# Kernel tuning notes

Hardware: AMD Instinct MI355X
Metric: run time of the kernel (lower is better)

Reference implementation:

```python
import jax, jax.numpy as jnp
import numpy as np

N_NODES = 50000
N_EDGES = 800000
HID = 96

def setup_inputs() -> dict:
    key = jax.random.key(0)
    ks = jax.random.split(key, 12)
    s = 1.0 / np.sqrt(HID)
    return {
        "x_feat": jax.random.normal(ks[0], (N_NODES, HID), jnp.float32),
        "bases": jax.random.normal(ks[1], (N_EDGES, HID), jnp.float32) * 0.1,
        "W_pre": jax.random.normal(ks[2], (HID, HID), jnp.float32) * s,
        "b_pre": jax.random.normal(ks[3], (HID,), jnp.float32) * s,
        "W1": jax.random.normal(ks[4], (HID, HID), jnp.float32) * s,
        "b1": jax.random.normal(ks[5], (HID,), jnp.float32) * s,
        "W2": jax.random.normal(ks[6], (HID, HID), jnp.float32) * s,
        "b2": jax.random.normal(ks[7], (HID,), jnp.float32) * s,
        "src": jax.random.randint(ks[8], (N_EDGES,), 0, N_NODES, jnp.int32),
        "dst": jax.random.randint(ks[9], (N_EDGES,), 0, N_NODES, jnp.int32),
    }

def _gelu(x):
    return jax.nn.gelu(x, approximate=False)  # torch nn.GELU default = erf

def reference(x_feat, bases, W_pre, b_pre, W1, b1, W2, b2, src, dst):
    n = x_feat.shape[0]
    # pre_ffn: Linear + GELU on node features
    h = _gelu(x_feat @ W_pre + b_pre)                      # [N, H]
    # update_all(u_mul_e('x','v'), sum): gather src feats, weight by edge bases, scatter-add to dst
    msg = h[src] * bases                                   # [E, H]
    aggr = jax.ops.segment_sum(msg, dst, num_segments=n)   # [N, H]
    # dropout is identity in eval mode (rate=0)
    x = x_feat + aggr                                      # residual 1
    y = _gelu(_gelu(x @ W1 + b1) @ W2 + b2)                # ffn (no batch norm)
    return x + y                                           # residual 2
```

## Files before the change

### kernel.cpp

```cpp
#include <hip/hip_runtime.h>

#define NODES 50000
#define EDGES 800000
#define H 96
#define CAP 64

typedef float floatx4 __attribute__((ext_vector_type(4)));
typedef unsigned short ushort8 __attribute__((ext_vector_type(8)));
typedef __bf16 bf16x8 __attribute__((ext_vector_type(8)));

static __device__ __forceinline__ unsigned short f2b(float f) {
    unsigned int u = __float_as_uint(f);
    u = u + 0x7fffu + ((u >> 16) & 1u);
    return (unsigned short)(u >> 16);
}
static __device__ __forceinline__ float b2f(unsigned short u) {
    return __uint_as_float(((unsigned int)u) << 16);
}
static __device__ __forceinline__ float gelu_erf(float x) {
    return 0.5f * x * (1.0f + erff(x * 0.70710678118654752f));
}
static __device__ __forceinline__ bf16x8 pack_bf8(floatx4 a, floatx4 b) {
    union { ushort8 u; bf16x8 v; } r;
    #pragma unroll
    for (int j = 0; j < 4; ++j) { r.u[j] = f2b(a[j]); r.u[4 + j] = f2b(b[j]); }
    return r.v;
}

__global__ __launch_bounds__(256) void gemm96_pre(
    const float* __restrict__ A,
    const float* __restrict__ W,
    const float* __restrict__ bias,
    unsigned short* __restrict__ outp,
    int* __restrict__ cursor,
    int* __restrict__ wctr,
    int nStrips)
{
    const int g = blockIdx.x * 256 + threadIdx.x;
    if (g < NODES) cursor[g] = g * CAP;
    if (g == 0) *wctr = 0;

    __shared__ unsigned short Wt[96][104];
    const int tid = threadIdx.x;
    #pragma unroll
    for (int j = 0; j < 36; ++j) {
        const int f = tid + 256 * j;
        const int k = f / 96, n = f - k * 96;
        Wt[n][k] = f2b(W[f]);
    }
    __syncthreads();

    const int lane = tid & 63;
    const int quad = lane >> 4;
    const int l16  = lane & 15;

    bf16x8 Bf[3][6];
    float  bv[6];
    #pragma unroll
    for (int ks = 0; ks < 3; ++ks)
        #pragma unroll
        for (int nt = 0; nt < 6; ++nt)
            Bf[ks][nt] = *(const bf16x8*)(&Wt[nt * 16 + l16][ks * 32 + quad * 8]);
    #pragma unroll
    for (int nt = 0; nt < 6; ++nt) bv[nt] = bias[nt * 16 + l16];

    const int gwave  = (blockIdx.x * 256 + tid) >> 6;
    const int nWaves = (gridDim.x * 256) >> 6;

    for (int strip = gwave; strip < nStrips; strip += nWaves) {
        const int row0 = strip * 16;
        const float* Ap = A + (size_t)(row0 + l16) * H + quad * 8;

        bf16x8 Af[3];
        #pragma unroll
        for (int ks = 0; ks < 3; ++ks) {
            const floatx4 a0 = *(const floatx4*)(Ap + ks * 32);
            const floatx4 a1 = *(const floatx4*)(Ap + ks * 32 + 4);
            Af[ks] = pack_bf8(a0, a1);
        }

        floatx4 acc[6];
        #pragma unroll
        for (int nt = 0; nt < 6; ++nt) acc[nt] = (floatx4){0.f, 0.f, 0.f, 0.f};
        #pragma unroll
        for (int ks = 0; ks < 3; ++ks)
            #pragma unroll
            for (int nt = 0; nt < 6; ++nt)
                acc[nt] = __builtin_amdgcn_mfma_f32_16x16x32_bf16(Af[ks], Bf[ks][nt], acc[nt], 0, 0, 0);

        #pragma unroll
        for (int nt = 0; nt < 6; ++nt) {
            const int col = nt * 16 + l16;
            #pragma unroll
            for (int r = 0; r < 4; ++r) {
                const int row = row0 + quad * 4 + r;
                outp[(size_t)row * H + col] = f2b(gelu_erf(acc[nt][r] + bv[nt]));
            }
        }
    }
}

__global__ __launch_bounds__(256) void build_csr2(
    const int* __restrict__ dst, const int* __restrict__ src,
    int* __restrict__ cursor, int2* __restrict__ csr)
{
    const int e = blockIdx.x * 256 + threadIdx.x;
    if (e < EDGES) {
        const int d = dst[e];
        const int p = atomicAdd(&cursor[d], 1);
        if (p < d * CAP + CAP) {
            int2 es; es.x = e; es.y = src[e];
            csr[p] = es;
        }
    }
}

__global__ __launch_bounds__(256, 2) void gather_ffn(
    const unsigned short* __restrict__ h,
    const float* __restrict__ bases,
    const int2* __restrict__ csr,
    const int* __restrict__ cursor,
    const float* __restrict__ x_feat,
    const float* __restrict__ W1, const float* __restrict__ b1,
    const float* __restrict__ W2, const float* __restrict__ b2,
    float* __restrict__ outp,
    int* __restrict__ wctr,
    int nStrips)
{
    __shared__ unsigned short Wt1[96][104];
    __shared__ unsigned short Wt2[96][104];
    __shared__ float          Xb[4][16][100];
    __shared__ unsigned short Tt[4][16][120];

    const int tid = threadIdx.x;
    #pragma unroll
    for (int j = 0; j < 36; ++j) {
        const int f = tid + 256 * j;
        const int k = f / 96, n = f - k * 96;
        Wt1[n][k] = f2b(W1[f]);
        Wt2[n][k] = f2b(W2[f]);
    }
    __syncthreads();

    const int lane = tid & 63;
    const int quad = lane >> 4;
    const int l16  = lane & 15;
    const int w    = tid >> 6;
    const int nd   = lane >> 2;
    const int seg  = lane & 3;
    const int c0   = seg * 24;

    float bv1[6], bv2[6];
    #pragma unroll
    for (int nt = 0; nt < 6; ++nt) {
        bv1[nt] = b1[nt * 16 + l16];
        bv2[nt] = b2[nt * 16 + l16];
    }

    for (;;) {
        int s;
        if (lane == 0) s = atomicAdd(wctr, 1);
        s = __shfl(s, 0);
        if (s >= nStrips) break;
        const int row0 = s * 16;

        const int node = row0 + nd;
        const int i0 = node * CAP;
        const int i1 = cursor[node];

        float acc[24];
        #pragma unroll
        for (int j = 0; j < 24; ++j) acc[j] = 0.f;
        for (int i = i0; i < i1; ++i) {
            const int2 es = csr[i];
            const float* bp = bases + (size_t)es.x * H + c0;
            const unsigned short* hp = h + (size_t)es.y * H + c0;
            floatx4 b[6]; ushort8 hv[3];
            #pragma unroll
            for (int j = 0; j < 6; ++j) b[j] = *(const floatx4*)(bp + 4 * j);
            #pragma unroll
            for (int j = 0; j < 3; ++j) hv[j] = *(const ushort8*)(hp + 8 * j);
            #pragma unroll
            for (int j = 0; j < 24; ++j)
                acc[j] = fmaf(b[j >> 2][j & 3], b2f(hv[j >> 3][j & 7]), acc[j]);
        }
        const float* xp = x_feat + (size_t)node * H + c0;
        #pragma unroll
        for (int j = 0; j < 6; ++j) {
            const floatx4 xv = *(const floatx4*)(xp + 4 * j);
            #pragma unroll
            for (int t = 0; t < 4; ++t) acc[4 * j + t] += xv[t];
        }
        #pragma unroll
        for (int j = 0; j < 6; ++j) {
            floatx4 v;
            #pragma unroll
            for (int t = 0; t < 4; ++t) v[t] = acc[4 * j + t];
            *(floatx4*)(&Xb[w][nd][c0 + 4 * j]) = v;
        }

        bf16x8 Af[3];
        #pragma unroll
        for (int ks = 0; ks < 3; ++ks) {
            const floatx4 a0 = *(const floatx4*)(&Xb[w][l16][ks * 32 + quad * 8]);
            const floatx4 a1 = *(const floatx4*)(&Xb[w][l16][ks * 32 + quad * 8 + 4]);
            Af[ks] = pack_bf8(a0, a1);
        }
        floatx4 facc[6];
        #pragma unroll
        for (int nt = 0; nt < 6; ++nt) facc[nt] = (floatx4){0.f, 0.f, 0.f, 0.f};
        #pragma unroll
        for (int ks = 0; ks < 3; ++ks)
            #pragma unroll
            for (int nt = 0; nt < 6; ++nt) {
                const bf16x8 Bf1 = *(const bf16x8*)(&Wt1[nt * 16 + l16][ks * 32 + quad * 8]);
                facc[nt] = __builtin_amdgcn_mfma_f32_16x16x32_bf16(Af[ks], Bf1, facc[nt], 0, 0, 0);
            }
        #pragma unroll
        for (int nt = 0; nt < 6; ++nt)
            #pragma unroll
            for (int r = 0; r < 4; ++r)
                Tt[w][quad * 4 + r][nt * 16 + l16] = f2b(gelu_erf(facc[nt][r] + bv1[nt]));

        bf16x8 Tf[3];
        #pragma unroll
        for (int ks = 0; ks < 3; ++ks)
            Tf[ks] = *(const bf16x8*)(&Tt[w][l16][ks * 32 + quad * 8]);
        #pragma unroll
        for (int nt = 0; nt < 6; ++nt) facc[nt] = (floatx4){0.f, 0.f, 0.f, 0.f};
        #pragma unroll
        for (int ks = 0; ks < 3; ++ks)
            #pragma unroll
            for (int nt = 0; nt < 6; ++nt) {
                const bf16x8 Bf2 = *(const bf16x8*)(&Wt2[nt * 16 + l16][ks * 32 + quad * 8]);
                facc[nt] = __builtin_amdgcn_mfma_f32_16x16x32_bf16(Tf[ks], Bf2, facc[nt], 0, 0, 0);
            }
        #pragma unroll
        for (int nt = 0; nt < 6; ++nt) {
            const int col = nt * 16 + l16;
            #pragma unroll
            for (int r = 0; r < 4; ++r) {
                const int row = row0 + quad * 4 + r;
                outp[(size_t)row * H + col] = Xb[w][quad * 4 + r][col]
                                            + gelu_erf(facc[nt][r] + bv2[nt]);
            }
        }
    }
}

extern "C" void kernel_launch(void* const* d_in, const int* in_sizes, int n_in,
                              void* d_out, int out_size, void* d_ws, size_t ws_size,
                              hipStream_t stream)
{
    const float* x_feat = (const float*)d_in[0];
    const float* bases  = (const float*)d_in[1];
    const float* W_pre  = (const float*)d_in[2];
    const float* b_pre  = (const float*)d_in[3];
    const float* W1     = (const float*)d_in[4];
    const float* b1     = (const float*)d_in[5];
    const float* W2     = (const float*)d_in[6];
    const float* b2     = (const float*)d_in[7];
    const int* src = (const int*)d_in[8];
    const int* dst = (const int*)d_in[9];

    char* ws = (char*)d_ws;
    int*            cursor = (int*)(ws);
    int*            wctr   = (int*)(ws + 200704);
    int2*           csr2   = (int2*)(ws + 1048576);
    unsigned short* h_bf   = (unsigned short*)(ws + 27262976);
    float*          out    = (float*)d_out;

    const int nStrips = NODES / 16;

    gemm96_pre<<<512, 256, 0, stream>>>(x_feat, W_pre, b_pre, h_bf, cursor, wctr, nStrips);
    build_csr2<<<(EDGES + 255) / 256, 256, 0, stream>>>(dst, src, cursor, csr2);
    gather_ffn<<<512, 256, 0, stream>>>(
        h_bf, bases, csr2, cursor, x_feat, W1, b1, W2, b2, out, wctr, nStrips);
}
```

Baseline: 569.9 us.

## Gather directly in MFMA operand layout, shrink scratch LDS, raise occupancy

The gather now assigns each lane the columns matching its MFMA A-fragment (node = l16, columns quad*8 + ks*32). The aggregated residual can then be packed straight into bf16 operands, with no LDS round trip. Per-wave scratch is reduced to one 3.5KB buffer that is reused for the residual transpose (done in two halves) and the XOR-swizzled GELU intermediate. That frees enough LDS for launch bounds of 3 blocks per SM and a 768-block grid. The edge loop is unrolled by two to expose more outstanding loads, and it clamps the edge count to CAP. The cost is more complex register use and some extra LDS stores and reads for the residual.

Result: faster. 557.7 us (-2.1%).

```diff
diff --git a/kernel.cpp b/kernel.cpp
--- a/kernel.cpp
+++ b/kernel.cpp
@@ -20,11 +20,17 @@
 static __device__ __forceinline__ float gelu_erf(float x) {
     return 0.5f * x * (1.0f + erff(x * 0.70710678118654752f));
 }
-static __device__ __forceinline__ bf16x8 pack_bf8(floatx4 a, floatx4 b) {
+static __device__ __forceinline__ bf16x8 pack_bf8(const float* a) {
     union { ushort8 u; bf16x8 v; } r;
     #pragma unroll
-    for (int j = 0; j < 4; ++j) { r.u[j] = f2b(a[j]); r.u[4 + j] = f2b(b[j]); }
+    for (int j = 0; j < 8; ++j) r.u[j] = f2b(a[j]);
     return r.v;
+}
+static __device__ __forceinline__ floatx4 vec4(const float* a) {
+    floatx4 v;
+    #pragma unroll
+    for (int j = 0; j < 4; ++j) v[j] = a[j];
+    return v;
 }
 
 __global__ __launch_bounds__(256) void gemm96_pre(
@@ -74,9 +80,12 @@
         bf16x8 Af[3];
         #pragma unroll
         for (int ks = 0; ks < 3; ++ks) {
+            float tmp[8];
             const floatx4 a0 = *(const floatx4*)(Ap + ks * 32);
             const floatx4 a1 = *(const floatx4*)(Ap + ks * 32 + 4);
-            Af[ks] = pack_bf8(a0, a1);
+            #pragma unroll
+            for (int j = 0; j < 4; ++j) { tmp[j] = a0[j]; tmp[4 + j] = a1[j]; }
+            Af[ks] = pack_bf8(tmp);
         }
 
         floatx4 acc[6];
@@ -115,7 +124,7 @@
     }
 }
 
-__global__ __launch_bounds__(256, 2) void gather_ffn(
+__global__ __launch_bounds__(256, 3) void gather_ffn(
     const unsigned short* __restrict__ h,
     const float* __restrict__ bases,
     const int2* __restrict__ csr,
@@ -129,8 +138,7 @@
 {
     __shared__ unsigned short Wt1[96][104];
     __shared__ unsigned short Wt2[96][104];
-    __shared__ float          Xb[4][16][100];
-    __shared__ unsigned short Tt[4][16][120];
+    __shared__ __align__(16) char Scr[4][3584];
 
     const int tid = threadIdx.x;
     #pragma unroll
@@ -146,9 +154,8 @@
     const int quad = lane >> 4;
     const int l16  = lane & 15;
     const int w    = tid >> 6;
-    const int nd   = lane >> 2;
-    const int seg  = lane & 3;
-    const int c0   = seg * 24;
+    float*          Sf = (float*)Scr[w];
+    unsigned short* St = (unsigned short*)Scr[w];
 
     float bv1[6], bv2[6];
     #pragma unroll
@@ -156,6 +163,9 @@
         bv1[nt] = b1[nt * 16 + l16];
         bv2[nt] = b2[nt * 16 + l16];
     }
+
+    const int wsw = quad << 3;
+    const int rsw = ((l16 >> 2) & 3) << 3;
 
     for (;;) {
         int s;
@@ -164,48 +174,97 @@
         if (s >= nStrips) break;
         const int row0 = s * 16;
 
-        const int node = row0 + nd;
+        const int node = row0 + l16;
         const int i0 = node * CAP;
-        const int i1 = cursor[node];
+        int i1 = cursor[node];
+        i1 = min(i1, i0 + CAP);
 
         float acc[24];
         #pragma unroll
         for (int j = 0; j < 24; ++j) acc[j] = 0.f;
-        for (int i = i0; i < i1; ++i) {
-            const int2 es = csr[i];
-            const float* bp = bases + (size_t)es.x * H + c0;
-            const unsigned short* hp = h + (size_t)es.y * H + c0;
-            floatx4 b[6]; ushort8 hv[3];
-            #pragma unroll
-            for (int j = 0; j < 6; ++j) b[j] = *(const floatx4*)(bp + 4 * j);
-            #pragma unroll
-            for (int j = 0; j < 3; ++j) hv[j] = *(const ushort8*)(hp + 8 * j);
-            #pragma unroll
-            for (int j = 0; j < 24; ++j)
-                acc[j] = fmaf(b[j >> 2][j & 3], b2f(hv[j >> 3][j & 7]), acc[j]);
-        }
-        const float* xp = x_feat + (size_t)node * H + c0;
-        #pragma unroll
-        for (int j = 0; j < 6; ++j) {
-            const floatx4 xv = *(const floatx4*)(xp + 4 * j);
-            #pragma unroll
-            for (int t = 0; t < 4; ++t) acc[4 * j + t] += xv[t];
-        }
-        #pragma unroll
-        for (int j = 0; j < 6; ++j) {
-            floatx4 v;
-            #pragma unroll
-            for (int t = 0; t < 4; ++t) v[t] = acc[4 * j + t];
-            *(floatx4*)(&Xb[w][nd][c0 + 4 * j]) = v;
-        }
+
+        int i = i0;
+        for (; i + 1 < i1; i += 2) {
+            const int2 ea = csr[i];
+            const int2 eb = csr[i + 1];
+            const float* bpa = bases + (size_t)ea.x * H + quad * 8;
+            const float* bpb = bases + (size_t)eb.x * H + quad * 8;
+            const unsigned short* hpa = h + (size_t)ea.y * H + quad * 8;
+            const unsigned short* hpb = h + (size_t)eb.y * H + quad * 8;
+            floatx4 ba[6], bb[6]; ushort8 hva[3], hvb[3];
+            #pragma unroll
+            for (int ks = 0; ks < 3; ++ks) {
+                ba[2*ks]   = *(const floatx4*)(bpa + ks * 32);
+                ba[2*ks+1] = *(const floatx4*)(bpa + ks * 32 + 4);
+                hva[ks]    = *(const ushort8*)(hpa + ks * 32);
+                bb[2*ks]   = *(const floatx4*)(bpb + ks * 32);
+                bb[2*ks+1] = *(const floatx4*)(bpb + ks * 32 + 4);
+                hvb[ks]    = *(const ushort8*)(hpb + ks * 32);
+            }
+            #pragma unroll
+            for (int ks = 0; ks < 3; ++ks)
+                #pragma unroll
+                for (int j = 0; j < 8; ++j) {
+                    acc[ks*8+j] = fmaf(ba[2*ks + (j>>2)][j&3], b2f(hva[ks][j]), acc[ks*8+j]);
+                    acc[ks*8+j] = fmaf(bb[2*ks + (j>>2)][j&3], b2f(hvb[ks][j]), acc[ks*8+j]);
+                }
+        }
+        if (i < i1) {
+            const int2 ea = csr[i];
+            const float* bpa = bases + (size_t)ea.x * H + quad * 8;
+            const unsigned short* hpa = h + (size_t)ea.y * H + quad * 8;
+            #pragma unroll
+            for (int ks = 0; ks < 3; ++ks) {
+                const floatx4 b0 = *(const floatx4*)(bpa + ks * 32);
+                const floatx4 b1v = *(const floatx4*)(bpa + ks * 32 + 4);
+                const ushort8 hv = *(const ushort8*)(hpa + ks * 32);
+                #pragma unroll
+                for (int j = 0; j < 4; ++j) {
+                    acc[ks*8+j]   = fmaf(b0[j],  b2f(hv[j]),     acc[ks*8+j]);
+                    acc[ks*8+4+j] = fmaf(b1v[j], b2f(hv[4+j]),   acc[ks*8+4+j]);
+                }
+            }
+        }
+
+        const float* xp = x_feat + (size_t)node * H + quad * 8;
+        #pragma unroll
+        for (int ks = 0; ks < 3; ++ks) {
+            const floatx4 x0 = *(const floatx4*)(xp + ks * 32);
+            const floatx4 x1 = *(const floatx4*)(xp + ks * 32 + 4);
+            #pragma unroll
+            for (int j = 0; j < 4; ++j) {
+                acc[ks*8+j]   += x0[j];
+                acc[ks*8+4+j] += x1[j];
+            }
+        }
+
+        *(floatx4*)&Sf[l16 * 52 + quad * 8]     = vec4(&acc[0]);
+        *(floatx4*)&Sf[l16 * 52 + quad * 8 + 4] = vec4(&acc[4]);
+        if (quad < 2) {
+            *(floatx4*)&Sf[l16 * 52 + 32 + quad * 8]     = vec4(&acc[8]);
+            *(floatx4*)&Sf[l16 * 52 + 32 + quad * 8 + 4] = vec4(&acc[12]);
+        }
+        float res[24];
+        #pragma unroll
+        for (int nt = 0; nt < 3; ++nt)
+            #pragma unroll
+            for (int r = 0; r < 4; ++r)
+                res[nt*4+r] = Sf[(quad*4+r) * 52 + nt*16 + l16];
+        if (quad >= 2) {
+            *(floatx4*)&Sf[l16 * 52 + (quad-2) * 8]     = vec4(&acc[8]);
+            *(floatx4*)&Sf[l16 * 52 + (quad-2) * 8 + 4] = vec4(&acc[12]);
+        }
+        *(floatx4*)&Sf[l16 * 52 + 16 + quad * 8]     = vec4(&acc[16]);
+        *(floatx4*)&Sf[l16 * 52 + 16 + quad * 8 + 4] = vec4(&acc[20]);
+        #pragma unroll
+        for (int nt = 3; nt < 6; ++nt)
+            #pragma unroll
+            for (int r = 0; r < 4; ++r)
+                res[nt*4+r] = Sf[(quad*4+r) * 52 + nt*16 + l16 - 48];
 
         bf16x8 Af[3];
         #pragma unroll
-        for (int ks = 0; ks < 3; ++ks) {
-            const floatx4 a0 = *(const floatx4*)(&Xb[w][l16][ks * 32 + quad * 8]);
-            const floatx4 a1 = *(const floatx4*)(&Xb[w][l16][ks * 32 + quad * 8 + 4]);
-            Af[ks] = pack_bf8(a0, a1);
-        }
+        for (int ks = 0; ks < 3; ++ks) Af[ks] = pack_bf8(&acc[ks * 8]);
         floatx4 facc[6];
         #pragma unroll
         for (int nt = 0; nt < 6; ++nt) facc[nt] = (floatx4){0.f, 0.f, 0.f, 0.f};
@@ -216,16 +275,18 @@
                 const bf16x8 Bf1 = *(const bf16x8*)(&Wt1[nt * 16 + l16][ks * 32 + quad * 8]);
                 facc[nt] = __builtin_amdgcn_mfma_f32_16x16x32_bf16(Af[ks], Bf1, facc[nt], 0, 0, 0);
             }
+
         #pragma unroll
         for (int nt = 0; nt < 6; ++nt)
             #pragma unroll
             for (int r = 0; r < 4; ++r)
-                Tt[w][quad * 4 + r][nt * 16 + l16] = f2b(gelu_erf(facc[nt][r] + bv1[nt]));
-
+                St[(quad*4+r) * 112 + ((nt*16 + l16) ^ wsw)] =
+                    f2b(gelu_erf(facc[nt][r] + bv1[nt]));
         bf16x8 Tf[3];
         #pragma unroll
         for (int ks = 0; ks < 3; ++ks)
-            Tf[ks] = *(const bf16x8*)(&Tt[w][l16][ks * 32 + quad * 8]);
+            Tf[ks] = *(const bf16x8*)(&St[l16 * 112 + ((ks*32 + quad*8) ^ rsw)]);
+
         #pragma unroll
         for (int nt = 0; nt < 6; ++nt) facc[nt] = (floatx4){0.f, 0.f, 0.f, 0.f};
         #pragma unroll
@@ -241,8 +302,7 @@
             #pragma unroll
             for (int r = 0; r < 4; ++r) {
                 const int row = row0 + quad * 4 + r;
-                outp[(size_t)row * H + col] = Xb[w][quad * 4 + r][col]
-                                            + gelu_erf(facc[nt][r] + bv2[nt]);
+                outp[(size_t)row * H + col] = res[nt*4+r] + gelu_erf(facc[nt][r] + bv2[nt]);
             }
         }
     }
@@ -274,6 +334,6 @@
 
     gemm96_pre<<<512, 256, 0, stream>>>(x_feat, W_pre, b_pre, h_bf, cursor, wctr, nStrips);
     build_csr2<<<(EDGES + 255) / 256, 256, 0, stream>>>(dst, src, cursor, csr2);
-    gather_ffn<<<512, 256, 0, stream>>>(
+    gather_ffn<<<768, 256, 0, stream>>>(
         h_bf, bases, csr2, cursor, x_feat, W1, b1, W2, b2, out, wctr, nStrips);
 }
```

## Split fused gather+FFN into a high-occupancy gather kernel and a separate FFN kernel

Applied to the files above, without the earlier changes.

The fused gather_ffn kernel is split in two. A new gather_nodes kernel uses 12 threads per node, each handling 8 features, with two edges per loop iteration and a launch bound of 8 blocks per CU, to raise memory-level parallelism on the random edge gathers. It writes the residual x to a global fp32 workspace, which ffn_dual then reads back, adding an extra write and read of the node features. The FFN stage swaps the atomic work counter for a static grid-stride loop and XOR-swizzles the intermediate shared tile to avoid bank conflicts.

Measured after the change: 535.1 us. 6.1% less time.

```diff
diff --git a/kernel.cpp b/kernel.cpp
--- a/kernel.cpp
+++ b/kernel.cpp
@@ -20,10 +20,10 @@
 static __device__ __forceinline__ float gelu_erf(float x) {
     return 0.5f * x * (1.0f + erff(x * 0.70710678118654752f));
 }
-static __device__ __forceinline__ bf16x8 pack_bf8(floatx4 a, floatx4 b) {
+static __device__ __forceinline__ bf16x8 pack_bf8(const float* a) {
     union { ushort8 u; bf16x8 v; } r;
     #pragma unroll
-    for (int j = 0; j < 4; ++j) { r.u[j] = f2b(a[j]); r.u[4 + j] = f2b(b[j]); }
+    for (int j = 0; j < 8; ++j) r.u[j] = f2b(a[j]);
     return r.v;
 }
 
@@ -33,12 +33,10 @@
     const float* __restrict__ bias,
     unsigned short* __restrict__ outp,
     int* __restrict__ cursor,
-    int* __restrict__ wctr,
     int nStrips)
 {
     const int g = blockIdx.x * 256 + threadIdx.x;
     if (g < NODES) cursor[g] = g * CAP;
-    if (g == 0) *wctr = 0;
 
     __shared__ unsigned short Wt[96][104];
     const int tid = threadIdx.x;
@@ -74,9 +72,12 @@
         bf16x8 Af[3];
         #pragma unroll
         for (int ks = 0; ks < 3; ++ks) {
+            float tmp[8];
             const floatx4 a0 = *(const floatx4*)(Ap + ks * 32);
             const floatx4 a1 = *(const floatx4*)(Ap + ks * 32 + 4);
-            Af[ks] = pack_bf8(a0, a1);
+            #pragma unroll
+            for (int j = 0; j < 4; ++j) { tmp[j] = a0[j]; tmp[4 + j] = a1[j]; }
+            Af[ks] = pack_bf8(tmp);
         }
 
         floatx4 acc[6];
@@ -115,22 +116,80 @@
     }
 }
 
-__global__ __launch_bounds__(256, 2) void gather_ffn(
+__global__ __launch_bounds__(256, 8) void gather_nodes(
     const unsigned short* __restrict__ h,
     const float* __restrict__ bases,
     const int2* __restrict__ csr,
     const int* __restrict__ cursor,
     const float* __restrict__ x_feat,
+    float* __restrict__ xb)
+{
+    const int t = blockIdx.x * 256 + threadIdx.x;
+    const int n = t / 12;
+    if (n >= NODES) return;
+    const int seg = t - n * 12;
+    const int so8 = seg * 8;
+    const int i0 = n * CAP;
+    const int i1 = min(cursor[n], i0 + CAP);
+
+    floatx4 acc0 = (floatx4){0.f, 0.f, 0.f, 0.f};
+    floatx4 acc1 = (floatx4){0.f, 0.f, 0.f, 0.f};
+
+    int i = i0;
+    for (; i + 1 < i1; i += 2) {
+        const int2 ea = csr[i];
+        const int2 eb = csr[i + 1];
+        const size_t eoa = (size_t)ea.x * H + so8;
+        const size_t eob = (size_t)eb.x * H + so8;
+        const floatx4 ba0 = *(const floatx4*)(bases + eoa);
+        const floatx4 ba1 = *(const floatx4*)(bases + eoa + 4);
+        const ushort8 hva = *(const ushort8*)(h + (size_t)ea.y * H + so8);
+        const floatx4 bb0 = *(const floatx4*)(bases + eob);
+        const floatx4 bb1 = *(const floatx4*)(bases + eob + 4);
+        const ushort8 hvb = *(const ushort8*)(h + (size_t)eb.y * H + so8);
+        #pragma unroll
+        for (int j = 0; j < 4; ++j) {
+            acc0[j] = fmaf(ba0[j], b2f(hva[j]),     acc0[j]);
+            acc1[j] = fmaf(ba1[j], b2f(hva[4 + j]), acc1[j]);
+        }
+        #pragma unroll
+        for (int j = 0; j < 4; ++j) {
+            acc0[j] = fmaf(bb0[j], b2f(hvb[j]),     acc0[j]);
+            acc1[j] = fmaf(bb1[j], b2f(hvb[4 + j]), acc1[j]);
+        }
+    }
+    if (i < i1) {
+        const int2 ea = csr[i];
+        const size_t eoa = (size_t)ea.x * H + so8;
+        const floatx4 ba0 = *(const floatx4*)(bases + eoa);
+        const floatx4 ba1 = *(const floatx4*)(bases + eoa + 4);
+        const ushort8 hva = *(const ushort8*)(h + (size_t)ea.y * H + so8);
+        #pragma unroll
+        for (int j = 0; j < 4; ++j) {
+            acc0[j] = fmaf(ba0[j], b2f(hva[j]),     acc0[j]);
+            acc1[j] = fmaf(ba1[j], b2f(hva[4 + j]), acc1[j]);
+        }
+    }
+
+    const size_t no = (size_t)n * H + so8;
+    const floatx4 x0 = *(const floatx4*)(x_feat + no);
+    const floatx4 x1 = *(const floatx4*)(x_feat + no + 4);
+    #pragma unroll
+    for (int j = 0; j < 4; ++j) { acc0[j] += x0[j]; acc1[j] += x1[j]; }
+    *(floatx4*)(xb + no)     = acc0;
+    *(floatx4*)(xb + no + 4) = acc1;
+}
+
+__global__ __launch_bounds__(256) void ffn_dual(
+    const float* __restrict__ A,
     const float* __restrict__ W1, const float* __restrict__ b1,
     const float* __restrict__ W2, const float* __restrict__ b2,
     float* __restrict__ outp,
-    int* __restrict__ wctr,
     int nStrips)
 {
     __shared__ unsigned short Wt1[96][104];
     __shared__ unsigned short Wt2[96][104];
-    __shared__ float          Xb[4][16][100];
-    __shared__ unsigned short Tt[4][16][120];
+    __shared__ unsigned short St[4][16][112];
 
     const int tid = threadIdx.x;
     #pragma unroll
@@ -146,9 +205,6 @@
     const int quad = lane >> 4;
     const int l16  = lane & 15;
     const int w    = tid >> 6;
-    const int nd   = lane >> 2;
-    const int seg  = lane & 3;
-    const int c0   = seg * 24;
 
     float bv1[6], bv2[6];
     #pragma unroll
@@ -157,54 +213,25 @@
         bv2[nt] = b2[nt * 16 + l16];
     }
 
-    for (;;) {
-        int s;
-        if (lane == 0) s = atomicAdd(wctr, 1);
-        s = __shfl(s, 0);
-        if (s >= nStrips) break;
-        const int row0 = s * 16;
-
-        const int node = row0 + nd;
-        const int i0 = node * CAP;
-        const int i1 = cursor[node];
-
-        float acc[24];
-        #pragma unroll
-        for (int j = 0; j < 24; ++j) acc[j] = 0.f;
-        for (int i = i0; i < i1; ++i) {
-            const int2 es = csr[i];
-            const float* bp = bases + (size_t)es.x * H + c0;
-            const unsigned short* hp = h + (size_t)es.y * H + c0;
-            floatx4 b[6]; ushort8 hv[3];
-            #pragma unroll
-            for (int j = 0; j < 6; ++j) b[j] = *(const floatx4*)(bp + 4 * j);
-            #pragma unroll
-            for (int j = 0; j < 3; ++j) hv[j] = *(const ushort8*)(hp + 8 * j);
-            #pragma unroll
-            for (int j = 0; j < 24; ++j)
-                acc[j] = fmaf(b[j >> 2][j & 3], b2f(hv[j >> 3][j & 7]), acc[j]);
-        }
-        const float* xp = x_feat + (size_t)node * H + c0;
-        #pragma unroll
-        for (int j = 0; j < 6; ++j) {
-            const floatx4 xv = *(const floatx4*)(xp + 4 * j);
-            #pragma unroll
-            for (int t = 0; t < 4; ++t) acc[4 * j + t] += xv[t];
-        }
-        #pragma unroll
-        for (int j = 0; j < 6; ++j) {
-            floatx4 v;
-            #pragma unroll
-            for (int t = 0; t < 4; ++t) v[t] = acc[4 * j + t];
-            *(floatx4*)(&Xb[w][nd][c0 + 4 * j]) = v;
-        }
+    const int wsw = quad << 3;
+    const int rsw = (l16 >> 2) << 3;
+
+    const int gwave  = (blockIdx.x * 256 + tid) >> 6;
+    const int nWaves = (gridDim.x * 256) >> 6;
+
+    for (int strip = gwave; strip < nStrips; strip += nWaves) {
+        const int row0 = strip * 16;
+        const float* Ap = A + (size_t)(row0 + l16) * H + quad * 8;
 
         bf16x8 Af[3];
         #pragma unroll
         for (int ks = 0; ks < 3; ++ks) {
-            const floatx4 a0 = *(const floatx4*)(&Xb[w][l16][ks * 32 + quad * 8]);
-            const floatx4 a1 = *(const floatx4*)(&Xb[w][l16][ks * 32 + quad * 8 + 4]);
-            Af[ks] = pack_bf8(a0, a1);
+            float tmp[8];
+            const floatx4 a0 = *(const floatx4*)(Ap + ks * 32);
+            const floatx4 a1 = *(const floatx4*)(Ap + ks * 32 + 4);
+            #pragma unroll
+            for (int j = 0; j < 4; ++j) { tmp[j] = a0[j]; tmp[4 + j] = a1[j]; }
+            Af[ks] = pack_bf8(tmp);
         }
         floatx4 facc[6];
         #pragma unroll
@@ -216,16 +243,18 @@
                 const bf16x8 Bf1 = *(const bf16x8*)(&Wt1[nt * 16 + l16][ks * 32 + quad * 8]);
                 facc[nt] = __builtin_amdgcn_mfma_f32_16x16x32_bf16(Af[ks], Bf1, facc[nt], 0, 0, 0);
             }
+
         #pragma unroll
         for (int nt = 0; nt < 6; ++nt)
             #pragma unroll
             for (int r = 0; r < 4; ++r)
-                Tt[w][quad * 4 + r][nt * 16 + l16] = f2b(gelu_erf(facc[nt][r] + bv1[nt]));
-
+                St[w][quad * 4 + r][(nt * 16 + l16) ^ wsw] =
+                    f2b(gelu_erf(facc[nt][r] + bv1[nt]));
         bf16x8 Tf[3];
         #pragma unroll
         for (int ks = 0; ks < 3; ++ks)
-            Tf[ks] = *(const bf16x8*)(&Tt[w][l16][ks * 32 + quad * 8]);
+            Tf[ks] = *(const bf16x8*)(&St[w][l16][(ks * 32 + quad * 8) ^ rsw]);
+
         #pragma unroll
         for (int nt = 0; nt < 6; ++nt) facc[nt] = (floatx4){0.f, 0.f, 0.f, 0.f};
         #pragma unroll
@@ -241,8 +270,8 @@
             #pragma unroll
             for (int r = 0; r < 4; ++r) {
                 const int row = row0 + quad * 4 + r;
-                outp[(size_t)row * H + col] = Xb[w][quad * 4 + r][col]
-                                            + gelu_erf(facc[nt][r] + bv2[nt]);
+                const size_t o = (size_t)row * H + col;
+                outp[o] = A[o] + gelu_erf(facc[nt][r] + bv2[nt]);
             }
         }
     }
@@ -265,15 +294,16 @@
 
     char* ws = (char*)d_ws;
     int*            cursor = (int*)(ws);
-    int*            wctr   = (int*)(ws + 200704);
     int2*           csr2   = (int2*)(ws + 1048576);
     unsigned short* h_bf   = (unsigned short*)(ws + 27262976);
+    float*          xb     = (float*)(ws + 37748736);
     float*          out    = (float*)d_out;
 
     const int nStrips = NODES / 16;
 
-    gemm96_pre<<<512, 256, 0, stream>>>(x_feat, W_pre, b_pre, h_bf, cursor, wctr, nStrips);
+    gemm96_pre<<<512, 256, 0, stream>>>(x_feat, W_pre, b_pre, h_bf, cursor, nStrips);
     build_csr2<<<(EDGES + 255) / 256, 256, 0, stream>>>(dst, src, cursor, csr2);
-    gather_ffn<<<512, 256, 0, stream>>>(
-        h_bf, bases, csr2, cursor, x_feat, W1, b1, W2, b2, out, wctr, nStrips);
-}
+    gather_nodes<<<(NODES * 12 + 255) / 256, 256, 0, stream>>>(
+        h_bf, bases, csr2, cursor, x_feat, xb);
+    ffn_dual<<<512, 256, 0, stream>>>(xb, W1, b1, W2, b2, out, nStrips);
+}
```
